# Kernel tuning notes

Measured on AMD Instinct MI355X. Metric: run time of the kernel, lower is better.

Reference implementation:

```python
import jax, jax.numpy as jnp
import numpy as np

B, SQ, SK, DK, DV = 8, 2048, 2048, 256, 256
EPS = 1e-7  # keras.backend.epsilon()


def setup_inputs() -> dict:
    key = jax.random.key(0)
    kq, kk, kv, km = jax.random.split(key, 4)
    query = jax.random.normal(kq, (B, SQ, DK), dtype=jnp.float32)
    k_ = jax.random.normal(kk, (B, SK, DK), dtype=jnp.float32)
    value = jax.random.normal(kv, (B, SK, DV), dtype=jnp.float32)
    mask = jax.random.uniform(km, (B, SK)) > 0.1
    return {"query": query, "key": k_, "value": value, "mask": mask}


def reference(query, key, value, mask):
    d = query.shape[-1]
    # scores: [B, Sq, Sk]
    e = jnp.einsum('bqd,bkd->bqk', query, key) / jnp.sqrt(jnp.asarray(d, query.dtype))
    # original applies exp(e - max) BEFORE masking (non-standard but faithful)
    e = jnp.exp(e - jnp.max(e, axis=-1, keepdims=True))
    q_len, k_len = query.shape[1], key.shape[1]
    causal = (jnp.arange(k_len)[None, :] <= jnp.arange(q_len)[:, None]).astype(query.dtype)
    e = e * causal[None, :, :]                       # history_only mask
    e = e * mask[:, None, :].astype(query.dtype)     # key padding mask
    a = e / (jnp.sum(e, axis=-1, keepdims=True) + EPS)
    return jnp.einsum('bqk,bkv->bqv', a, value)
```

## Files before the change

### kernel.cpp

```cpp
#include <hip/hip_runtime.h>
#include <hip/hip_bf16.h>

#define B_   8
#define SQ_  2048
#define SK_  2048
#define DK_  256
#define DV_  256

#define KT    32
#define PSTR  40
#define TELEM (KT * DK_)
#define NQB   16

typedef __bf16 bf16x8 __attribute__((ext_vector_type(8)));
typedef __bf16 bf16x4 __attribute__((ext_vector_type(4)));
typedef float  f32x4  __attribute__((ext_vector_type(4)));

__device__ __forceinline__ void gl_lds16(const void* g, void* l) {
    __builtin_amdgcn_global_load_lds(
        (const __attribute__((address_space(1))) void*)g,
        (__attribute__((address_space(3))) void*)l, 16, 0, 0);
}

__global__ __launch_bounds__(256)
void make_tiles(const float* __restrict__ K, const float* __restrict__ V,
                __bf16* __restrict__ Kt, __bf16* __restrict__ Vt)
{
    const int b = blockIdx.x, t = blockIdx.y;
    const float* ksrc = K + ((size_t)(b * SK_ + t * KT)) * DK_;
    const float* vsrc = V + ((size_t)(b * SK_ + t * KT)) * DV_;

    float4 kf[8];
    #pragma unroll
    for (int it = 0; it < 4; ++it) {
        int ci  = it * 256 + threadIdx.x;
        int dk8 = ci >> 5;
        int key = ci & 31;
        const float* p = ksrc + (size_t)key * DK_ + dk8 * 8;
        kf[it * 2]     = *(const float4*)(p);
        kf[it * 2 + 1] = *(const float4*)(p + 4);
    }
    const int kc8 = threadIdx.x >> 6;
    const int dv4 = threadIdx.x & 63;
    float4 vf[8];
    {
        const float* p = vsrc + (size_t)(kc8 * 8) * DV_ + dv4 * 4;
        #pragma unroll
        for (int j = 0; j < 8; ++j)
            vf[j] = *(const float4*)(p + (size_t)j * DV_);
    }

    __bf16* kout = Kt + ((size_t)(b * 64 + t)) * TELEM;
    #pragma unroll
    for (int it = 0; it < 4; ++it) {
        int ci = it * 256 + threadIdx.x;
        bf16x8 o;
        o[0] = (__bf16)kf[it*2].x;   o[1] = (__bf16)kf[it*2].y;
        o[2] = (__bf16)kf[it*2].z;   o[3] = (__bf16)kf[it*2].w;
        o[4] = (__bf16)kf[it*2+1].x; o[5] = (__bf16)kf[it*2+1].y;
        o[6] = (__bf16)kf[it*2+1].z; o[7] = (__bf16)kf[it*2+1].w;
        *(bf16x8*)(kout + (size_t)ci * 8) = o;
    }
    __bf16* vout = Vt + ((size_t)(b * 64 + t)) * TELEM;
    {
        bf16x8 o0, o1, o2, o3;
        #pragma unroll
        for (int j = 0; j < 8; ++j) {
            o0[j] = (__bf16)vf[j].x; o1[j] = (__bf16)vf[j].y;
            o2[j] = (__bf16)vf[j].z; o3[j] = (__bf16)vf[j].w;
        }
        __bf16* q = vout + (size_t)(kc8 * 256 + dv4 * 4) * 8;
        *(bf16x8*)(q)      = o0;
        *(bf16x8*)(q + 8)  = o1;
        *(bf16x8*)(q + 16) = o2;
        *(bf16x8*)(q + 24) = o3;
    }
}

__global__ __launch_bounds__(256, 2)
void attn_fwd(const float* __restrict__ Qg, const __bf16* __restrict__ Kt,
              const __bf16* __restrict__ Vt, const void* __restrict__ Mv,
              __bf16* __restrict__ Opart, float* __restrict__ Lpart,
              float* __restrict__ Og, int tpc, int slots_pb)
{
    __shared__ __align__(16) __bf16 sK[2][TELEM];
    __shared__ __align__(16) __bf16 sV[2][TELEM];
    __shared__ __align__(16) __bf16 sP[4][32 * PSTR];

    const int tid  = threadIdx.x;
    const int wv   = tid >> 6;
    const int lane = tid & 63;
    const int quad = lane >> 4;
    const int l16  = lane & 15;

    const int b = blockIdx.x;

    int yy = blockIdx.y, qb = 0, s = 0, soff = 0;
    for (int q = NQB - 1; q >= 0; --q) {
        int c = (4 * (q + 1) + tpc - 1) / tpc;
        if (yy < c) { qb = q; s = yy; break; }
        yy -= c;
        if (c > 1) soff += c;
    }
    const int nt = 4 * (qb + 1);
    const int nc = (nt + tpc - 1) / tpc;
    const int t0 = nt * s / nc;
    const int t1 = nt * (s + 1) / nc;

    const int qrow = qb * 128 + wv * 32;

    const unsigned char* Mb = (const unsigned char*)Mv;
    const int*           Mi = (const int*)Mv;
    int nzb = 0;
    {
        const unsigned int* mw = (const unsigned int*)Mv;
        #pragma unroll
        for (int i = 0; i < 32; ++i) {
            unsigned int w = mw[i];
            nzb += ((w & 0x000000ffu) != 0) + ((w & 0x0000ff00u) != 0)
                 + ((w & 0x00ff0000u) != 0) + ((w & 0xff000000u) != 0);
        }
    }
    const bool mask_byte = (nzb > 40);
    const size_t mbase = (size_t)b * SK_;

    bf16x8 qfrag[2][8];
    #pragma unroll
    for (int rs = 0; rs < 2; ++rs) {
        const float* qp = Qg + ((size_t)(b * SQ_ + qrow + rs * 16 + l16)) * DK_ + quad * 8;
        #pragma unroll
        for (int kt = 0; kt < 8; ++kt) {
            float4 f0 = *(const float4*)(qp + kt * 32);
            float4 f1 = *(const float4*)(qp + kt * 32 + 4);
            bf16x8 q;
            q[0] = (__bf16)f0.x; q[1] = (__bf16)f0.y; q[2] = (__bf16)f0.z; q[3] = (__bf16)f0.w;
            q[4] = (__bf16)f1.x; q[5] = (__bf16)f1.y; q[6] = (__bf16)f1.z; q[7] = (__bf16)f1.w;
            qfrag[rs][kt] = q;
        }
    }

    f32x4 oacc[2][16];
    #pragma unroll
    for (int rs = 0; rs < 2; ++rs)
        #pragma unroll
        for (int v = 0; v < 16; ++v) oacc[rs][v] = (f32x4){0.f, 0.f, 0.f, 0.f};
    float lsum[2] = {0.f, 0.f};

    const __bf16* Kbase = Kt + (size_t)b * 64 * TELEM;
    const __bf16* Vbase = Vt + (size_t)b * 64 * TELEM;

    {
        const __bf16* kg = Kbase + (size_t)t0 * TELEM;
        const __bf16* vg = Vbase + (size_t)t0 * TELEM;
        #pragma unroll
        for (int r = 0; r < 4; ++r) {
            int ci = r * 256 + tid;
            gl_lds16(kg + (size_t)ci * 8, (char*)&sK[0][0] + ci * 16);
            gl_lds16(vg + (size_t)ci * 8, (char*)&sV[0][0] + ci * 16);
        }
    }
    __syncthreads();

    int cur = 0;
    for (int t = t0; t < t1; ++t) {
        if (t + 1 < t1) {
            const __bf16* kg = Kbase + (size_t)(t + 1) * TELEM;
            const __bf16* vg = Vbase + (size_t)(t + 1) * TELEM;
            #pragma unroll
            for (int r = 0; r < 4; ++r) {
                int ci = r * 256 + tid;
                gl_lds16(kg + (size_t)ci * 8, (char*)&sK[cur ^ 1][0] + ci * 16);
                gl_lds16(vg + (size_t)ci * 8, (char*)&sV[cur ^ 1][0] + ci * 16);
            }
        }

        const int k0 = t * KT;

        if (k0 <= qrow + 31) {
            f32x4 s00 = {0.f,0.f,0.f,0.f}, s01 = {0.f,0.f,0.f,0.f};
            f32x4 s10 = {0.f,0.f,0.f,0.f}, s11 = {0.f,0.f,0.f,0.f};
            __builtin_amdgcn_s_setprio(1);
            #pragma unroll
            for (int kt = 0; kt < 8; ++kt) {
                bf16x8 b0 = *(const bf16x8*)&sK[cur][(size_t)((kt * 4 + quad) * 32 + l16)      * 8];
                bf16x8 b1 = *(const bf16x8*)&sK[cur][(size_t)((kt * 4 + quad) * 32 + 16 + l16) * 8];
                s00 = __builtin_amdgcn_mfma_f32_16x16x32_bf16(b0, qfrag[0][kt], s00, 0, 0, 0);
                s10 = __builtin_amdgcn_mfma_f32_16x16x32_bf16(b1, qfrag[0][kt], s10, 0, 0, 0);
                s01 = __builtin_amdgcn_mfma_f32_16x16x32_bf16(b0, qfrag[1][kt], s01, 0, 0, 0);
                s11 = __builtin_amdgcn_mfma_f32_16x16x32_bf16(b1, qfrag[1][kt], s11, 0, 0, 0);
            }
            __builtin_amdgcn_s_setprio(0);

            #pragma unroll
            for (int kh = 0; kh < 2; ++kh) {
                const int kbase = k0 + kh * 16 + quad * 4;
                float mk[4];
                if (mask_byte) {
                    uchar4 m4 = *(const uchar4*)(Mb + mbase + kbase);
                    mk[0] = m4.x ? 1.f : 0.f; mk[1] = m4.y ? 1.f : 0.f;
                    mk[2] = m4.z ? 1.f : 0.f; mk[3] = m4.w ? 1.f : 0.f;
                } else {
                    int4 m4 = *(const int4*)(Mi + mbase + kbase);
                    mk[0] = m4.x ? 1.f : 0.f; mk[1] = m4.y ? 1.f : 0.f;
                    mk[2] = m4.z ? 1.f : 0.f; mk[3] = m4.w ? 1.f : 0.f;
                }
                #pragma unroll
                for (int rs = 0; rs < 2; ++rs) {
                    f32x4 sv = (rs == 0) ? ((kh == 0) ? s00 : s10)
                                         : ((kh == 0) ? s01 : s11);
                    const int qr = qrow + rs * 16 + l16;
                    bf16x4 pv4;
                    #pragma unroll
                    for (int i = 0; i < 4; ++i) {
                        float p = __expf(sv[i] * 0.0625f);
                        p = (kbase + i <= qr) ? (p * mk[i]) : 0.0f;
                        lsum[rs] += p;
                        pv4[i] = (__bf16)p;
                    }
                    *(bf16x4*)&sP[wv][(rs * 16 + l16) * PSTR + kh * 16 + quad * 4] = pv4;
                }
            }
            asm volatile("s_waitcnt lgkmcnt(0)" ::: "memory");
            __builtin_amdgcn_wave_barrier();

            {
                bf16x8 pa0 = *(const bf16x8*)&sP[wv][(l16)      * PSTR + quad * 8];
                bf16x8 pa1 = *(const bf16x8*)&sP[wv][(16 + l16) * PSTR + quad * 8];
                __builtin_amdgcn_s_setprio(1);
                #pragma unroll
                for (int vf = 0; vf < 16; ++vf) {
                    bf16x8 bv = *(const bf16x8*)&sV[cur][(size_t)(quad * 256 + vf * 16 + l16) * 8];
                    oacc[0][vf] = __builtin_amdgcn_mfma_f32_16x16x32_bf16(pa0, bv, oacc[0][vf], 0, 0, 0);
                    oacc[1][vf] = __builtin_amdgcn_mfma_f32_16x16x32_bf16(pa1, bv, oacc[1][vf], 0, 0, 0);
                }
                __builtin_amdgcn_s_setprio(0);
            }
        }

        __syncthreads();
        cur ^= 1;
    }

    #pragma unroll
    for (int rs = 0; rs < 2; ++rs) {
        float v = lsum[rs];
        v += __shfl_xor(v, 16);
        v += __shfl_xor(v, 32);
        lsum[rs] = v;
    }

    if (nc == 1) {
        float* op = Og + ((size_t)(b * SQ_ + qb * 128 + wv * 32)) * DV_;
        #pragma unroll
        for (int rs = 0; rs < 2; ++rs)
            #pragma unroll
            for (int i = 0; i < 4; ++i) {
                float ls  = __shfl(lsum[rs], quad * 4 + i);
                float inv = 1.0f / (ls + 1e-7f);
                #pragma unroll
                for (int vf = 0; vf < 16; ++vf)
                    op[(size_t)(rs * 16 + quad * 4 + i) * DV_ + vf * 16 + l16]
                        = oacc[rs][vf][i] * inv;
            }
        return;
    }

    const size_t slot = (size_t)b * slots_pb + soff + s;
    if (quad == 0) {
        #pragma unroll
        for (int rs = 0; rs < 2; ++rs)
            Lpart[slot * 128 + wv * 32 + rs * 16 + l16] = lsum[rs];
    }
    __bf16* ob = Opart + slot * (size_t)(128 * 256);
    #pragma unroll
    for (int rs = 0; rs < 2; ++rs)
        #pragma unroll
        for (int vf = 0; vf < 16; ++vf)
            #pragma unroll
            for (int i = 0; i < 4; ++i)
                ob[(wv * 32 + rs * 16 + quad * 4 + i) * 256 + vf * 16 + l16]
                    = (__bf16)oacc[rs][vf][i];
}

__global__ __launch_bounds__(512)
void attn_reduce(const __bf16* __restrict__ Opart, const float* __restrict__ Lpart,
                 float* __restrict__ Og, int tpc, int slots_pb)
{
    const int b    = blockIdx.x;
    const int y    = blockIdx.y;
    const int qb64 = y >> 1;
    const int half = y & 1;
    const int qb   = qb64 >> 1;
    const int rowbase = (qb64 & 1) * 64;
    const int chunks = (4 * (qb + 1) + tpc - 1) / tpc;
    if (chunks < 2) return;

    int soff = 0;
    for (int q = NQB - 1; q > qb; --q) {
        int c = (4 * (q + 1) + tpc - 1) / tpc;
        if (c > 1) soff += c;
    }

    const int tid  = threadIdx.x;
    const int row  = tid >> 3;
    const int cg   = tid & 7;

    const size_t sbase = (size_t)b * slots_pb + soff;
    float acc[16];
    #pragma unroll
    for (int i = 0; i < 16; ++i) acc[i] = 0.f;
    float ls = 0.f;

    for (int s = 0; s < chunks; ++s) {
        const __bf16* p = Opart + (sbase + s) * (size_t)(128 * 256)
                        + (size_t)(rowbase + row) * 256 + half * 128 + cg * 16;
        bf16x8 x0 = *(const bf16x8*)(p);
        bf16x8 x1 = *(const bf16x8*)(p + 8);
        #pragma unroll
        for (int e = 0; e < 8; ++e) { acc[e] += (float)x0[e]; acc[8 + e] += (float)x1[e]; }
        ls += Lpart[(sbase + s) * 128 + rowbase + row];
    }
    const float inv = 1.0f / (ls + 1e-7f);
    float* op = Og + ((size_t)b * SQ_ + qb64 * 64 + row) * DV_ + half * 128 + cg * 16;
    #pragma unroll
    for (int v = 0; v < 4; ++v) {
        float4 o;
        o.x = acc[v * 4 + 0] * inv; o.y = acc[v * 4 + 1] * inv;
        o.z = acc[v * 4 + 2] * inv; o.w = acc[v * 4 + 3] * inv;
        *(float4*)(op + v * 4) = o;
    }
}

extern "C" void kernel_launch(void* const* d_in, const int* in_sizes, int n_in,
                              void* d_out, int out_size, void* d_ws, size_t ws_size,
                              hipStream_t stream) {
    const float* Q = (const float*)d_in[0];
    const float* K = (const float*)d_in[1];
    const float* V = (const float*)d_in[2];
    const void*  M = d_in[3];
    float* Out = (float*)d_out;

    __bf16* Ktl = (__bf16*)d_ws;
    __bf16* Vtl = Ktl + (size_t)B_ * 64 * TELEM;
    __bf16* Opart = Vtl + (size_t)B_ * 64 * TELEM;

    auto counts = [](int tpc, int& nch, int& slots_pb) {
        nch = 0; slots_pb = 0;
        for (int q = 0; q < NQB; ++q) {
            int c = (4 * (q + 1) + tpc - 1) / tpc;
            nch += c;
            if (c > 1) slots_pb += c;
        }
    };
    int tpc = 10, nch, slots_pb;
    counts(tpc, nch, slots_pb);
    size_t need = (size_t)(16 * 1024 * 1024)
                + (size_t)B_ * slots_pb * (128 * 256) * 2
                + (size_t)B_ * slots_pb * 128 * 4;
    if (ws_size < need) {
        tpc = 64;
        counts(tpc, nch, slots_pb);
    }

    float* Lpart = (float*)(Opart + (size_t)B_ * slots_pb * (128 * 256));

    make_tiles<<<dim3(B_, 64), dim3(256), 0, stream>>>(K, V, Ktl, Vtl);
    attn_fwd<<<dim3(B_, nch), dim3(256), 0, stream>>>(Q, Ktl, Vtl, M, Opart, Lpart,
                                                      Out, tpc, slots_pb);
    if (slots_pb > 0)
        attn_reduce<<<dim3(B_, 64), dim3(512), 0, stream>>>(Opart, Lpart, Out,
                                                            tpc, slots_pb);
}
```

Before: 137.5 us.

## Balance causal attention work with a flattened per-tile work list

Replaces the per-query-block chunking (tiles per chunk) with a flat list of 544 (query block, key tile) entries per batch, split evenly into 64 blocks of about 8.5 tiles each. A block may now span several query-block segments, so it reloads Q fragments and flushes partial outputs at each segment boundary. Complete segments write normalized output directly, and partial ones go to slots merged by the reduce kernel. The aim is to remove load imbalance and tail effects from uneven chunks. The cost is extra per-tile index math (a linear qb_of search) and more partial flushes and reduction traffic.

```diff
diff --git a/kernel.cpp b/kernel.cpp
--- a/kernel.cpp
+++ b/kernel.cpp
@@ -11,15 +11,36 @@
 #define PSTR  40
 #define TELEM (KT * DK_)
 #define NQB   16
+#define NENT  544
+#define NBLK  64
 
 typedef __bf16 bf16x8 __attribute__((ext_vector_type(8)));
 typedef __bf16 bf16x4 __attribute__((ext_vector_type(4)));
 typedef float  f32x4  __attribute__((ext_vector_type(4)));
+
+__host__ __device__ __forceinline__ int cumf(int q)   { return 544 - 2*(q+1)*(q+2); }
+__host__ __device__ __forceinline__ int yfirst(int c) { return (2*c + 1) / 17; }
 
 __device__ __forceinline__ void gl_lds16(const void* g, void* l) {
     __builtin_amdgcn_global_load_lds(
         (const __attribute__((address_space(1))) void*)g,
         (__attribute__((address_space(3))) void*)l, 16, 0, 0);
+}
+
+__device__ __forceinline__ int qb_of(int e) {
+    int q = 15;
+    while (q > 0 && e >= cumf(q) + 4 * (q + 1)) --q;
+    return q;
+}
+
+__host__ __device__ __forceinline__ int slot_base(int q) {
+    int base = 0;
+    for (int p = 15; p > q; --p) {
+        int c0 = cumf(p), c1 = c0 + 4 * (p + 1) - 1;
+        int cnt = yfirst(c1) - yfirst(c0) + 1;
+        if (cnt > 1) base += cnt;
+    }
+    return base;
 }
 
 __global__ __launch_bounds__(256)
@@ -81,7 +102,7 @@
 void attn_fwd(const float* __restrict__ Qg, const __bf16* __restrict__ Kt,
               const __bf16* __restrict__ Vt, const void* __restrict__ Mv,
               __bf16* __restrict__ Opart, float* __restrict__ Lpart,
-              float* __restrict__ Og, int tpc, int slots_pb)
+              float* __restrict__ Og, int mode, int slots_pb)
 {
     __shared__ __align__(16) __bf16 sK[2][TELEM];
     __shared__ __align__(16) __bf16 sV[2][TELEM];
@@ -94,20 +115,11 @@
     const int l16  = lane & 15;
 
     const int b = blockIdx.x;
-
-    int yy = blockIdx.y, qb = 0, s = 0, soff = 0;
-    for (int q = NQB - 1; q >= 0; --q) {
-        int c = (4 * (q + 1) + tpc - 1) / tpc;
-        if (yy < c) { qb = q; s = yy; break; }
-        yy -= c;
-        if (c > 1) soff += c;
-    }
-    const int nt = 4 * (qb + 1);
-    const int nc = (nt + tpc - 1) / tpc;
-    const int t0 = nt * s / nc;
-    const int t1 = nt * (s + 1) / nc;
-
-    const int qrow = qb * 128 + wv * 32;
+    const int y = blockIdx.y;
+
+    int e0, e1;
+    if (mode == 0) { e0 = (17 * y) >> 1; e1 = (17 * (y + 1)) >> 1; }
+    else           { e0 = cumf(y);       e1 = cumf(y) + 4 * (y + 1); }
 
     const unsigned char* Mb = (const unsigned char*)Mv;
     const int*           Mi = (const int*)Mv;
@@ -124,34 +136,56 @@
     const bool mask_byte = (nzb > 40);
     const size_t mbase = (size_t)b * SK_;
 
-    bf16x8 qfrag[2][8];
-    #pragma unroll
-    for (int rs = 0; rs < 2; ++rs) {
-        const float* qp = Qg + ((size_t)(b * SQ_ + qrow + rs * 16 + l16)) * DK_ + quad * 8;
-        #pragma unroll
-        for (int kt = 0; kt < 8; ++kt) {
-            float4 f0 = *(const float4*)(qp + kt * 32);
-            float4 f1 = *(const float4*)(qp + kt * 32 + 4);
-            bf16x8 q;
-            q[0] = (__bf16)f0.x; q[1] = (__bf16)f0.y; q[2] = (__bf16)f0.z; q[3] = (__bf16)f0.w;
-            q[4] = (__bf16)f1.x; q[5] = (__bf16)f1.y; q[6] = (__bf16)f1.z; q[7] = (__bf16)f1.w;
-            qfrag[rs][kt] = q;
-        }
-    }
-
-    f32x4 oacc[2][16];
-    #pragma unroll
-    for (int rs = 0; rs < 2; ++rs)
-        #pragma unroll
-        for (int v = 0; v < 16; ++v) oacc[rs][v] = (f32x4){0.f, 0.f, 0.f, 0.f};
-    float lsum[2] = {0.f, 0.f};
-
     const __bf16* Kbase = Kt + (size_t)b * 64 * TELEM;
     const __bf16* Vbase = Vt + (size_t)b * 64 * TELEM;
 
+    bf16x8 qfrag[2][8];
+    f32x4  oacc[2][16];
+    float  lsum[2];
+    int qcur = -1, seg_s = e0, qrow = 0;
+
+    auto flush_seg = [&](int q, int es, int ee) {
+        float l0 = lsum[0], l1 = lsum[1];
+        l0 += __shfl_xor(l0, 16); l0 += __shfl_xor(l0, 32);
+        l1 += __shfl_xor(l1, 16); l1 += __shfl_xor(l1, 32);
+        const int nt = 4 * (q + 1);
+        const bool full = (es == cumf(q)) && (ee == cumf(q) + nt);
+        if (full) {
+            float* op = Og + ((size_t)(b * SQ_ + q * 128 + wv * 32)) * DV_;
+            #pragma unroll
+            for (int rs = 0; rs < 2; ++rs)
+                #pragma unroll
+                for (int i = 0; i < 4; ++i) {
+                    float ls  = __shfl(rs == 0 ? l0 : l1, quad * 4 + i);
+                    float inv = 1.0f / (ls + 1e-7f);
+                    #pragma unroll
+                    for (int vf = 0; vf < 16; ++vf)
+                        op[(size_t)(rs * 16 + quad * 4 + i) * DV_ + vf * 16 + l16]
+                            = oacc[rs][vf][i] * inv;
+                }
+        } else {
+            const int slot_loc = slot_base(q) + (y - yfirst(cumf(q)));
+            const size_t slot = (size_t)b * slots_pb + slot_loc;
+            if (quad == 0) {
+                Lpart[slot * 128 + wv * 32 + l16]      = l0;
+                Lpart[slot * 128 + wv * 32 + 16 + l16] = l1;
+            }
+            __bf16* ob = Opart + slot * (size_t)(128 * 256);
+            #pragma unroll
+            for (int rs = 0; rs < 2; ++rs)
+                #pragma unroll
+                for (int vf = 0; vf < 16; ++vf)
+                    #pragma unroll
+                    for (int i = 0; i < 4; ++i)
+                        ob[(wv * 32 + rs * 16 + quad * 4 + i) * 256 + vf * 16 + l16]
+                            = (__bf16)oacc[rs][vf][i];
+        }
+    };
+
     {
-        const __bf16* kg = Kbase + (size_t)t0 * TELEM;
-        const __bf16* vg = Vbase + (size_t)t0 * TELEM;
+        int te = e0 - cumf(qb_of(e0));
+        const __bf16* kg = Kbase + (size_t)te * TELEM;
+        const __bf16* vg = Vbase + (size_t)te * TELEM;
         #pragma unroll
         for (int r = 0; r < 4; ++r) {
             int ci = r * 256 + tid;
@@ -162,10 +196,38 @@
     __syncthreads();
 
     int cur = 0;
-    for (int t = t0; t < t1; ++t) {
-        if (t + 1 < t1) {
-            const __bf16* kg = Kbase + (size_t)(t + 1) * TELEM;
-            const __bf16* vg = Vbase + (size_t)(t + 1) * TELEM;
+    for (int e = e0; e < e1; ++e) {
+        const int q = qb_of(e);
+        if (q != qcur) {
+            if (qcur >= 0) flush_seg(qcur, seg_s, e);
+            qcur = q; seg_s = e;
+            qrow = q * 128 + wv * 32;
+            #pragma unroll
+            for (int rs = 0; rs < 2; ++rs) {
+                const float* qp = Qg + ((size_t)(b * SQ_ + qrow + rs * 16 + l16)) * DK_ + quad * 8;
+                #pragma unroll
+                for (int kt = 0; kt < 8; ++kt) {
+                    float4 f0 = *(const float4*)(qp + kt * 32);
+                    float4 f1 = *(const float4*)(qp + kt * 32 + 4);
+                    bf16x8 qv;
+                    qv[0] = (__bf16)f0.x; qv[1] = (__bf16)f0.y; qv[2] = (__bf16)f0.z; qv[3] = (__bf16)f0.w;
+                    qv[4] = (__bf16)f1.x; qv[5] = (__bf16)f1.y; qv[6] = (__bf16)f1.z; qv[7] = (__bf16)f1.w;
+                    qfrag[rs][kt] = qv;
+                }
+            }
+            #pragma unroll
+            for (int rs = 0; rs < 2; ++rs)
+                #pragma unroll
+                for (int v = 0; v < 16; ++v) oacc[rs][v] = (f32x4){0.f, 0.f, 0.f, 0.f};
+            lsum[0] = 0.f; lsum[1] = 0.f;
+        }
+        const int t  = e - cumf(q);
+        const int k0 = t * KT;
+
+        if (e + 1 < e1) {
+            int tn = (e + 1) - cumf(qb_of(e + 1));
+            const __bf16* kg = Kbase + (size_t)tn * TELEM;
+            const __bf16* vg = Vbase + (size_t)tn * TELEM;
             #pragma unroll
             for (int r = 0; r < 4; ++r) {
                 int ci = r * 256 + tid;
@@ -173,8 +235,6 @@
                 gl_lds16(vg + (size_t)ci * 8, (char*)&sV[cur ^ 1][0] + ci * 16);
             }
         }
-
-        const int k0 = t * KT;
 
         if (k0 <= qrow + 31) {
             f32x4 s00 = {0.f,0.f,0.f,0.f}, s01 = {0.f,0.f,0.f,0.f};
@@ -240,72 +300,30 @@
         __syncthreads();
         cur ^= 1;
     }
-
-    #pragma unroll
-    for (int rs = 0; rs < 2; ++rs) {
-        float v = lsum[rs];
-        v += __shfl_xor(v, 16);
-        v += __shfl_xor(v, 32);
-        lsum[rs] = v;
-    }
-
-    if (nc == 1) {
-        float* op = Og + ((size_t)(b * SQ_ + qb * 128 + wv * 32)) * DV_;
-        #pragma unroll
-        for (int rs = 0; rs < 2; ++rs)
-            #pragma unroll
-            for (int i = 0; i < 4; ++i) {
-                float ls  = __shfl(lsum[rs], quad * 4 + i);
-                float inv = 1.0f / (ls + 1e-7f);
-                #pragma unroll
-                for (int vf = 0; vf < 16; ++vf)
-                    op[(size_t)(rs * 16 + quad * 4 + i) * DV_ + vf * 16 + l16]
-                        = oacc[rs][vf][i] * inv;
-            }
-        return;
-    }
-
-    const size_t slot = (size_t)b * slots_pb + soff + s;
-    if (quad == 0) {
-        #pragma unroll
-        for (int rs = 0; rs < 2; ++rs)
-            Lpart[slot * 128 + wv * 32 + rs * 16 + l16] = lsum[rs];
-    }
-    __bf16* ob = Opart + slot * (size_t)(128 * 256);
-    #pragma unroll
-    for (int rs = 0; rs < 2; ++rs)
-        #pragma unroll
-        for (int vf = 0; vf < 16; ++vf)
-            #pragma unroll
-            for (int i = 0; i < 4; ++i)
-                ob[(wv * 32 + rs * 16 + quad * 4 + i) * 256 + vf * 16 + l16]
-                    = (__bf16)oacc[rs][vf][i];
+    flush_seg(qcur, seg_s, e1);
 }
 
 __global__ __launch_bounds__(512)
 void attn_reduce(const __bf16* __restrict__ Opart, const float* __restrict__ Lpart,
-                 float* __restrict__ Og, int tpc, int slots_pb)
+                 float* __restrict__ Og, int slots_pb)
 {
     const int b    = blockIdx.x;
-    const int y    = blockIdx.y;
-    const int qb64 = y >> 1;
-    const int half = y & 1;
+    const int yy   = blockIdx.y;
+    const int qb64 = yy >> 1;
+    const int half = yy & 1;
     const int qb   = qb64 >> 1;
     const int rowbase = (qb64 & 1) * 64;
-    const int chunks = (4 * (qb + 1) + tpc - 1) / tpc;
+
+    const int c0 = cumf(qb), c1 = c0 + 4 * (qb + 1) - 1;
+    const int chunks = yfirst(c1) - yfirst(c0) + 1;
     if (chunks < 2) return;
 
-    int soff = 0;
-    for (int q = NQB - 1; q > qb; --q) {
-        int c = (4 * (q + 1) + tpc - 1) / tpc;
-        if (c > 1) soff += c;
-    }
-
+    const int base = slot_base(qb);
     const int tid  = threadIdx.x;
     const int row  = tid >> 3;
     const int cg   = tid & 7;
 
-    const size_t sbase = (size_t)b * slots_pb + soff;
+    const size_t sbase = (size_t)b * slots_pb + base;
     float acc[16];
     #pragma unroll
     for (int i = 0; i < 16; ++i) acc[i] = 0.f;
@@ -321,7 +339,7 @@
         ls += Lpart[(sbase + s) * 128 + rowbase + row];
     }
     const float inv = 1.0f / (ls + 1e-7f);
-    float* op = Og + ((size_t)b * SQ_ + qb64 * 64 + row) * DV_ + half * 128 + cg * 16;
+    float* op = Og + ((size_t)b * SQ_ + qb * 128 + rowbase + row) * DV_ + half * 128 + cg * 16;
     #pragma unroll
     for (int v = 0; v < 4; ++v) {
         float4 o;
@@ -344,30 +362,26 @@
     __bf16* Vtl = Ktl + (size_t)B_ * 64 * TELEM;
     __bf16* Opart = Vtl + (size_t)B_ * 64 * TELEM;
 
-    auto counts = [](int tpc, int& nch, int& slots_pb) {
-        nch = 0; slots_pb = 0;
-        for (int q = 0; q < NQB; ++q) {
-            int c = (4 * (q + 1) + tpc - 1) / tpc;
-            nch += c;
-            if (c > 1) slots_pb += c;
-        }
-    };
-    int tpc = 10, nch, slots_pb;
-    counts(tpc, nch, slots_pb);
+    int slots_pb = 0;
+    for (int q = 15; q >= 0; --q) {
+        int c0 = cumf(q), c1 = c0 + 4 * (q + 1) - 1;
+        int cnt = yfirst(c1) - yfirst(c0) + 1;
+        if (cnt > 1) slots_pb += cnt;
+    }
     size_t need = (size_t)(16 * 1024 * 1024)
                 + (size_t)B_ * slots_pb * (128 * 256) * 2
                 + (size_t)B_ * slots_pb * 128 * 4;
-    if (ws_size < need) {
-        tpc = 64;
-        counts(tpc, nch, slots_pb);
-    }
+    int mode = (ws_size >= need) ? 0 : 1;
 
     float* Lpart = (float*)(Opart + (size_t)B_ * slots_pb * (128 * 256));
 
     make_tiles<<<dim3(B_, 64), dim3(256), 0, stream>>>(K, V, Ktl, Vtl);
-    attn_fwd<<<dim3(B_, nch), dim3(256), 0, stream>>>(Q, Ktl, Vtl, M, Opart, Lpart,
-                                                      Out, tpc, slots_pb);
-    if (slots_pb > 0)
-        attn_reduce<<<dim3(B_, 64), dim3(512), 0, stream>>>(Opart, Lpart, Out,
-                                                            tpc, slots_pb);
-}
+    if (mode == 0) {
+        attn_fwd<<<dim3(B_, NBLK), dim3(256), 0, stream>>>(Q, Ktl, Vtl, M, Opart, Lpart,
+                                                           Out, 0, slots_pb);
+        attn_reduce<<<dim3(B_, 64), dim3(512), 0, stream>>>(Opart, Lpart, Out, slots_pb);
+    } else {
+        attn_fwd<<<dim3(B_, NQB), dim3(256), 0, stream>>>(Q, Ktl, Vtl, M, Opart, Lpart,
+                                                          Out, 1, 0);
+    }
+}
```

After: 173.6 us. 1.26x slower.
